# Kernel tuning notes

Measured on AMD Instinct MI355X. Metric: run time of the kernel, lower is better.

## Reference

```python
import jax, jax.numpy as jnp
import numpy as np

N, M, T_STEPS = 32, 64, 20000  # t = T/dt = 200/0.01
DT = 0.01
SQRT_DT = DT ** 0.5


def setup_inputs() -> dict:
    key = jax.random.key(0)
    k1, k2 = jax.random.split(key)
    # theta ~ U(lower, upper) per the module's prior (4-param variant)
    lower = jnp.array([0.5, 0.1, 0.1, 0.0], dtype=jnp.float32)
    upper = jnp.array([1.5, 3.0, 0.6, 4.0], dtype=jnp.float32)
    theta = lower + (upper - lower) * jax.random.uniform(k1, (N, 4), dtype=jnp.float32)
    noise = jax.random.normal(k2, (N, M, T_STEPS), dtype=jnp.float32)
    return {"theta": theta, "noise": noise}


def reference(theta, noise):
    # Euler-Maruyama OU recurrence: x_{i+1} = x_i + gamma*(mu - x_i)*dt + sigma*sqrt(dt)*eps_i
    n, m, t = noise.shape
    gamma = theta[:, 0][:, None]  # [n,1] broadcasts over m
    mu = theta[:, 1][:, None]
    sigma = theta[:, 2][:, None]
    x0 = jnp.broadcast_to(theta[:, 3][:, None], (n, m))

    eps_t = jnp.moveaxis(noise, -1, 0)  # [t, n, m] for scan

    def step(x, eps):
        x_new = x + gamma * (mu - x) * DT + sigma * SQRT_DT * eps
        return x_new, x_new

    _, xs = jax.lax.scan(step, x0, eps_t)  # xs: [t, n, m] == x[:, :, 1:]
    return jnp.moveaxis(xs, 0, -1)  # [n, m, t]
```

## Files before the change

### kernel.cpp

```cpp
#include <hip/hip_runtime.h>


#define T_STEPS 20000
#define M_PATHS 64
#define CHUNK   32
#define TILE    (64 * CHUNK)
#define NTILES  ((T_STEPS + TILE - 1) / TILE)
#define DT      0.01f
#define SQRT_DT 0.1f

__global__ __launch_bounds__(256) void ou_scan_kernel(
    const float* __restrict__ theta,
    const float* __restrict__ noise,
    float* __restrict__ out)
{
    const int wave  = threadIdx.x >> 6;
    const int lane  = threadIdx.x & 63;
    const int chain = blockIdx.x * 4 + wave;
    const int n     = chain / M_PATHS;

    const float gamma = theta[n * 4 + 0];
    const float mu    = theta[n * 4 + 1];
    const float sigma = theta[n * 4 + 2];
    float carry       = theta[n * 4 + 3];

    const float a    = 1.0f - gamma * DT;
    const float gmdt = gamma * mu * DT;
    const float ssd  = sigma * SQRT_DT;
    const float a2  = a * a;
    const float a4  = a2 * a2;
    const float a8  = a4 * a4;
    const float a16 = a8 * a8;
    const float a32 = a16 * a16;

    const float* __restrict__ np_ = noise + (size_t)chain * T_STEPS;
    float* __restrict__       op_ = out   + (size_t)chain * T_STEPS;

    float4 cur[8], nxt[8];

    {
        const int e0 = lane * CHUNK;
        const bool act = (e0 + CHUNK <= T_STEPS);
        #pragma unroll
        for (int k = 0; k < 8; ++k)
            cur[k] = act ? *(const float4*)(np_ + e0 + 4 * k)
                         : make_float4(0.f, 0.f, 0.f, 0.f);
    }

    for (int tb = 0; tb < NTILES; ++tb) {
        {
            const int ne0 = (tb + 1) * TILE + lane * CHUNK;
            const bool act = (tb + 1 < NTILES) && (ne0 + CHUNK <= T_STEPS);
            #pragma unroll
            for (int k = 0; k < 8; ++k)
                nxt[k] = act ? *(const float4*)(np_ + ne0 + 4 * k)
                             : make_float4(0.f, 0.f, 0.f, 0.f);
        }

        const int  base = tb * TILE + lane * CHUNK;
        const bool cact = (base + CHUNK <= T_STEPS);

        float p = 0.0f;
        #pragma unroll
        for (int k = 0; k < 8; ++k) {
            const float4 c = cur[k];
            p = fmaf(p, a, fmaf(ssd, c.x, gmdt));
            p = fmaf(p, a, fmaf(ssd, c.y, gmdt));
            p = fmaf(p, a, fmaf(ssd, c.z, gmdt));
            p = fmaf(p, a, fmaf(ssd, c.w, gmdt));
        }

        float A = cact ? a32 : 1.0f;
        float B = cact ? p   : 0.0f;

        #pragma unroll
        for (int d = 1; d < 64; d <<= 1) {
            const float pA = __shfl_up(A, d);
            const float pB = __shfl_up(B, d);
            if (lane >= d) {
                B = fmaf(A, pB, B);
                A = A * pA;
            }
        }

        float Aex = __shfl_up(A, 1);
        float Bex = __shfl_up(B, 1);
        if (lane == 0) { Aex = 1.0f; Bex = 0.0f; }
        float x = fmaf(Aex, carry, Bex);

        const float A63 = __shfl(A, 63);
        const float B63 = __shfl(B, 63);
        carry = fmaf(A63, carry, B63);

        if (cact) {
            #pragma unroll
            for (int k = 0; k < 8; ++k) {
                const float4 c = cur[k];
                float4 o;
                x = fmaf(a, x, fmaf(ssd, c.x, gmdt)); o.x = x;
                x = fmaf(a, x, fmaf(ssd, c.y, gmdt)); o.y = x;
                x = fmaf(a, x, fmaf(ssd, c.z, gmdt)); o.z = x;
                x = fmaf(a, x, fmaf(ssd, c.w, gmdt)); o.w = x;
                *(float4*)(op_ + base + 4 * k) = o;
            }
        }

        #pragma unroll
        for (int k = 0; k < 8; ++k) cur[k] = nxt[k];
    }
}

extern "C" void kernel_launch(void* const* d_in, const int* in_sizes, int n_in,
                              void* d_out, int out_size, void* d_ws, size_t ws_size,
                              hipStream_t stream) {
    const float* theta = (const float*)d_in[0];
    const float* noise = (const float*)d_in[1];
    float* out = (float*)d_out;

    const int chains = in_sizes[1] / T_STEPS;
    const int blocks = chains / 4;
    ou_scan_kernel<<<blocks, 256, 0, stream>>>(theta, noise, out);
}
```

Baseline: 308.4 us.

## Split each chain across a full block with cross-wave scan via shared memory

Each 256-thread block now handles one chain instead of four, so four waves cooperate on a tile of 8192 steps. Per-wave affine maps are combined through a double-buffered shared-memory array after a __syncthreads, and the software prefetch of the next tile is removed. This gives 2048 blocks instead of 512, raising parallelism and cutting the number of serial tiles per chain from 10 to 3. The cost is a block barrier per tile and the loss of explicit load/compute overlap.

```diff
diff --git a/kernel.cpp b/kernel.cpp
--- a/kernel.cpp
+++ b/kernel.cpp
@@ -4,19 +4,22 @@
 #define T_STEPS 20000
 #define M_PATHS 64
 #define CHUNK   32
-#define TILE    (64 * CHUNK)
+#define TILE    (256 * CHUNK)
 #define NTILES  ((T_STEPS + TILE - 1) / TILE)
 #define DT      0.01f
 #define SQRT_DT 0.1f
 
-__global__ __launch_bounds__(256) void ou_scan_kernel(
+__global__ __launch_bounds__(256, 8) void ou_scan_kernel(
     const float* __restrict__ theta,
     const float* __restrict__ noise,
     float* __restrict__ out)
 {
-    const int wave  = threadIdx.x >> 6;
-    const int lane  = threadIdx.x & 63;
-    const int chain = blockIdx.x * 4 + wave;
+    __shared__ float2 wmap[2][4];
+
+    const int t    = threadIdx.x;
+    const int wave = t >> 6;
+    const int lane = t & 63;
+    const int chain = blockIdx.x;
     const int n     = chain / M_PATHS;
 
     const float gamma = theta[n * 4 + 0];
@@ -36,29 +39,15 @@
     const float* __restrict__ np_ = noise + (size_t)chain * T_STEPS;
     float* __restrict__       op_ = out   + (size_t)chain * T_STEPS;
 
-    float4 cur[8], nxt[8];
+    for (int tb = 0; tb < NTILES; ++tb) {
+        const int  base = tb * TILE + t * CHUNK;
+        const bool act  = (base + CHUNK <= T_STEPS);
 
-    {
-        const int e0 = lane * CHUNK;
-        const bool act = (e0 + CHUNK <= T_STEPS);
+        float4 cur[8];
         #pragma unroll
         for (int k = 0; k < 8; ++k)
-            cur[k] = act ? *(const float4*)(np_ + e0 + 4 * k)
+            cur[k] = act ? *(const float4*)(np_ + base + 4 * k)
                          : make_float4(0.f, 0.f, 0.f, 0.f);
-    }
-
-    for (int tb = 0; tb < NTILES; ++tb) {
-        {
-            const int ne0 = (tb + 1) * TILE + lane * CHUNK;
-            const bool act = (tb + 1 < NTILES) && (ne0 + CHUNK <= T_STEPS);
-            #pragma unroll
-            for (int k = 0; k < 8; ++k)
-                nxt[k] = act ? *(const float4*)(np_ + ne0 + 4 * k)
-                             : make_float4(0.f, 0.f, 0.f, 0.f);
-        }
-
-        const int  base = tb * TILE + lane * CHUNK;
-        const bool cact = (base + CHUNK <= T_STEPS);
 
         float p = 0.0f;
         #pragma unroll
@@ -70,8 +59,8 @@
             p = fmaf(p, a, fmaf(ssd, c.w, gmdt));
         }
 
-        float A = cact ? a32 : 1.0f;
-        float B = cact ? p   : 0.0f;
+        float A = act ? a32 : 1.0f;
+        float B = act ? p   : 0.0f;
 
         #pragma unroll
         for (int d = 1; d < 64; d <<= 1) {
@@ -86,13 +75,25 @@
         float Aex = __shfl_up(A, 1);
         float Bex = __shfl_up(B, 1);
         if (lane == 0) { Aex = 1.0f; Bex = 0.0f; }
-        float x = fmaf(Aex, carry, Bex);
 
-        const float A63 = __shfl(A, 63);
-        const float B63 = __shfl(B, 63);
-        carry = fmaf(A63, carry, B63);
+        if (lane == 63) wmap[tb & 1][wave] = make_float2(A, B);
+        __syncthreads();
 
-        if (cact) {
+        float EA = 1.0f, EB = 0.0f;
+        float pEA = 1.0f, pEB = 0.0f;
+        #pragma unroll
+        for (int w = 0; w < 4; ++w) {
+            if (w == wave) { pEA = EA; pEB = EB; }
+            const float2 m = wmap[tb & 1][w];
+            EB = fmaf(m.x, EB, m.y);
+            EA = m.x * EA;
+        }
+
+        const float xw = fmaf(pEA, carry, pEB);
+        float x        = fmaf(Aex, xw, Bex);
+        carry          = fmaf(EA, carry, EB);
+
+        if (act) {
             #pragma unroll
             for (int k = 0; k < 8; ++k) {
                 const float4 c = cur[k];
@@ -104,9 +105,6 @@
                 *(float4*)(op_ + base + 4 * k) = o;
             }
         }
-
-        #pragma unroll
-        for (int k = 0; k < 8; ++k) cur[k] = nxt[k];
     }
 }
 
@@ -118,6 +116,5 @@
     float* out = (float*)d_out;
 
     const int chains = in_sizes[1] / T_STEPS;
-    const int blocks = chains / 4;
-    ou_scan_kernel<<<blocks, 256, 0, stream>>>(theta, noise, out);
+    ou_scan_kernel<<<chains, 256, 0, stream>>>(theta, noise, out);
 }
```

Result: slower. 336.9 us (+9.2%).
